# Optimization experiments

Measured on AMD Instinct MI355X. Metric: run time of the kernel, lower is better.

The kernel has to match this reference:

```python
import jax, jax.numpy as jnp
import numpy as np

HEADS = 16
DIM_HEAD = 32
WSZ = 7
DIM = 512
INNER = HEADS * DIM_HEAD
LN_EPS = 1e-5


def setup_inputs() -> dict:
    key = jax.random.key(0)
    ks = jax.random.split(key, 9)
    b, H, W = 16, 56, 56
    x = jax.random.normal(ks[0], (b, DIM, H, W), dtype=jnp.float32)
    w_qkv = jax.random.normal(ks[1], (INNER * 3, DIM), dtype=jnp.float32) * (DIM ** -0.5)
    window_tokens = jax.random.normal(ks[2], (DIM,), dtype=jnp.float32)
    ln_w = jnp.ones((DIM_HEAD,), dtype=jnp.float32)
    ln_b = jnp.zeros((DIM_HEAD,), dtype=jnp.float32)
    w_qk = jax.random.normal(ks[3], (INNER * 2, INNER), dtype=jnp.float32) * (INNER ** -0.5)
    b_qk = jnp.zeros((INNER * 2,), dtype=jnp.float32)
    w_out = jax.random.normal(ks[4], (DIM, INNER), dtype=jnp.float32) * (INNER ** -0.5)
    b_out = jnp.zeros((DIM,), dtype=jnp.float32)
    return {"x": x, "w_qkv": w_qkv, "window_tokens": window_tokens,
            "ln_w": ln_w, "ln_b": ln_b, "w_qk": w_qk, "b_qk": b_qk,
            "w_out": w_out, "b_out": b_out}


def reference(x, w_qkv, window_tokens, ln_w, ln_b, w_qk, b_qk, w_out, b_out):
    b, c, H, W = x.shape
    h, d, wsz = HEADS, DIM_HEAD, WSZ
    X, Y = H // wsz, W // wsz
    nw = X * Y            # number of windows per image
    n = wsz * wsz         # tokens per window (49)
    scale = d ** -0.5

    # b c (X w1) (Y w2) -> (b X Y) c (w1 w2)
    xw = x.reshape(b, c, X, wsz, Y, wsz).transpose(0, 2, 4, 1, 3, 5).reshape(b * nw, c, n)
    wt = jnp.broadcast_to(window_tokens[None, :, None], (b * nw, c, 1))
    xc = jnp.concatenate([wt, xw], axis=-1)                 # [BW, c, n+1]

    qkv = jnp.einsum('oc,bcn->bon', w_qkv, xc)              # 1x1 conv, no bias
    q, k, v = jnp.split(qkv, 3, axis=1)
    def to_heads(t):
        return t.reshape(t.shape[0], h, d, n + 1).transpose(0, 1, 3, 2)  # [BW,h,n+1,d]
    q, k, v = to_heads(q), to_heads(k), to_heads(v)

    dots = jnp.einsum('bhid,bhjd->bhij', q * scale, k)      # [BW,h,50,50]
    attn = jax.nn.softmax(dots, axis=-1)
    out = jnp.einsum('bhij,bhjd->bhid', attn, v)            # [BW,h,50,d]

    wtok = out[:, :, 0].reshape(b, nw, h, d).transpose(0, 2, 1, 3)          # [b,h,nw,d]
    wfm = out[:, :, 1:].reshape(b, nw, h, n, d).transpose(0, 2, 1, 3, 4)    # [b,h,nw,n,d]

    # window_tokens_to_qk: LayerNorm(d) -> GELU -> conv1d(inner, 2*inner)
    mu = wtok.mean(-1, keepdims=True)
    var = wtok.var(-1, keepdims=True)
    normed = (wtok - mu) / jnp.sqrt(var + LN_EPS) * ln_w + ln_b
    g = jax.nn.gelu(normed, approximate=False)
    gf = g.transpose(0, 1, 3, 2).reshape(b, h * d, nw)      # b h n c -> b (h c) n
    qk = jnp.einsum('oc,bcn->bon', w_qk, gf) + b_qk[None, :, None]
    qk = qk.reshape(b, h, 2 * d, nw).transpose(0, 1, 3, 2)  # [b,h,nw,2d]
    w_q, w_k = qk[..., :d], qk[..., d:]

    w_dots = jnp.einsum('bhid,bhjd->bhij', w_q * scale, w_k)  # [b,h,nw,nw]
    w_attn = jax.nn.softmax(w_dots, axis=-1)
    agg = jnp.einsum('bhij,bhjnd->bhind', w_attn, wfm)        # [b,h,nw,n,d]

    # b h (X Y) (w1 w2) d -> b (h d) (X w1) (Y w2)
    fmap = agg.reshape(b, h, X, Y, wsz, wsz, d).transpose(0, 1, 6, 2, 4, 3, 5).reshape(b, h * d, H, W)
    return jnp.einsum('oc,bchw->bohw', w_out, fmap) + b_out[None, :, None, None]
```

## Files before the change

kernel.cpp:

```cpp
#include <hip/hip_runtime.h>
#include <math.h>

#define SCALE_D 0.17677669529663687f

typedef __attribute__((ext_vector_type(8))) short short8;
typedef __attribute__((ext_vector_type(4))) float f32x4;

__device__ __forceinline__ unsigned short f2bf(float f) {
  unsigned u = __builtin_bit_cast(unsigned, f);
  unsigned r = u + 0x7FFF + ((u >> 16) & 1);
  return (unsigned short)(r >> 16);
}
__device__ __forceinline__ float bf2f(unsigned short h) {
  unsigned u = ((unsigned)h) << 16;
  return __builtin_bit_cast(float, u);
}
__device__ __forceinline__ void gload16(const void* g, void* l) {
  __builtin_amdgcn_global_load_lds((const __attribute__((address_space(1))) unsigned int*)g,
                                   (__attribute__((address_space(3))) unsigned int*)l,
                                   16, 0, 0);
}

__global__ __launch_bounds__(256) void k_split(const float* __restrict__ src,
                                               unsigned short* __restrict__ hi,
                                               unsigned short* __restrict__ lo, int n) {
  int i = blockIdx.x * 256 + threadIdx.x;
  if (i < n) {
    float v = src[i];
    unsigned short h = f2bf(v);
    hi[i] = h;
    lo[i] = f2bf(v - bf2f(h));
  }
}

__global__ __launch_bounds__(256) void k_build_xcT(const float* __restrict__ x,
                                                   const float* __restrict__ wtok,
                                                   unsigned short* __restrict__ Thi,
                                                   unsigned short* __restrict__ Tlo,
                                                   int bb0) {
  const int cblk = blockIdx.x;
  const int h    = blockIdx.y;
  const int bbL  = blockIdx.z;
  const int bb   = bb0 + bbL;
  const int tid  = threadIdx.x;
  const int c0   = cblk * 64;
  if (h == 56) {
    for (int e = tid; e < 4096; e += 256) {
      int wl = e >> 6, cl = e & 63;
      float v = wtok[c0 + cl];
      unsigned short hv = f2bf(v);
      long idx = ((long)(bbL * 64 + wl) * 50) * 512 + c0 + cl;
      Thi[idx] = hv;
      Tlo[idx] = f2bf(v - bf2f(hv));
    }
    return;
  }
  __shared__ unsigned short shi[64][57], slo[64][57];
  const int Xw = h / 7, r7 = h % 7;
  for (int e = tid; e < 3584; e += 256) {
    int cl = e / 56, w = e - cl * 56;
    float v = x[((long)(bb * 512 + c0 + cl) * 56 + h) * 56 + w];
    unsigned short hv = f2bf(v);
    shi[cl][w] = hv;
    slo[cl][w] = f2bf(v - bf2f(hv));
  }
  __syncthreads();
  for (int e = tid; e < 3584; e += 256) {
    int row = e >> 6, cl = e & 63;
    int Yw = row / 7, c7 = row - Yw * 7;
    long trow = (long)(bbL * 64 + Xw * 8 + Yw) * 50 + 1 + r7 * 7 + c7;
    Thi[trow * 512 + c0 + cl] = shi[cl][row];
    Tlo[trow * 512 + c0 + cl] = slo[cl][row];
  }
}

template <int PACK>
__global__ __launch_bounds__(256, 2) void k_gemm_mfma(
    const unsigned short* __restrict__ Ahi, const unsigned short* __restrict__ Alo,
    const unsigned short* __restrict__ Bhi, const unsigned short* __restrict__ Blo,
    float* __restrict__ C, const float* __restrict__ bias,
    int NC, int brow_stride, long c_stride) {
  __shared__ unsigned short lds[2][4][128][32];
  const int tid = threadIdx.x;
  const int wv = tid >> 6, lane = tid & 63;

  const int gy = gridDim.y;
  const int nwg = gridDim.x * gy;
  int hw = blockIdx.y * gridDim.x + blockIdx.x;
  int flat;
  {
    int q = nwg >> 3, r = nwg & 7;
    int xcd = hw & 7, k = hw >> 3;
    int start = (xcd < r) ? xcd * (q + 1) : r * (q + 1) + (xcd - r) * q;
    flat = start + k;
  }
  const int bx = flat / gy, by = flat % gy;
  const int m0 = by * 128, n0 = bx * 128;
  const long brow0 = (long)blockIdx.z * brow_stride + n0;
  C += (long)blockIdx.z * c_stride;

  const int wr = wv >> 1, wc = wv & 1;
  const int lr = lane & 15, kb = lane >> 4;
  const int srow = lane >> 2, sju = lane & 3;
  const int sswz = (sju ^ ((srow >> 1) & 3)) * 8;
  const int rswz = (lr >> 1) & 3;

  f32x4 acc[4][4];
#pragma unroll
  for (int i = 0; i < 4; ++i)
#pragma unroll
    for (int j = 0; j < 4; ++j) {
      f32x4 z = {0.f, 0.f, 0.f, 0.f};
      acc[i][j] = z;
    }

  auto STAGE = [&](int buf, int k0) {
#pragma unroll
    for (int it = 0; it < 2; ++it) {
      const int rloc = (wv * 2 + it) * 16;
      const int r = rloc + srow;
      const long ga = (long)(m0 + r) * 512 + k0 + sswz;
      gload16(Ahi + ga, &lds[buf][0][rloc][0]);
      gload16(Alo + ga, &lds[buf][1][rloc][0]);
      const long gb = (brow0 + r) * 512 + k0 + sswz;
      gload16(Bhi + gb, &lds[buf][2][rloc][0]);
      gload16(Blo + gb, &lds[buf][3][rloc][0]);
    }
  };

  STAGE(0, 0);
  int cur = 0;
  for (int t = 0; t < 16; ++t) {
    if (t < 15) STAGE(cur ^ 1, (t + 1) * 32);
    if (t < 15) {
      asm volatile("s_waitcnt vmcnt(8)" ::: "memory");
    } else {
      asm volatile("s_waitcnt vmcnt(0)" ::: "memory");
    }
    __builtin_amdgcn_s_barrier();
    asm volatile("" ::: "memory");
    short8 ah[4], al[4], bh[4], bl[4];
#pragma unroll
    for (int f = 0; f < 4; ++f) {
      int ra = wr * 64 + f * 16 + lr;
      int ca = (kb ^ rswz) * 8;
      ah[f] = *(const short8*)&lds[cur][0][ra][ca];
      al[f] = *(const short8*)&lds[cur][1][ra][ca];
      int rb = wc * 64 + f * 16 + lr;
      bh[f] = *(const short8*)&lds[cur][2][rb][ca];
      bl[f] = *(const short8*)&lds[cur][3][rb][ca];
    }
#pragma unroll
    for (int i = 0; i < 4; ++i)
#pragma unroll
      for (int j = 0; j < 4; ++j) {
        acc[i][j] = __builtin_amdgcn_mfma_f32_16x16x32_bf16(ah[i], bh[j], acc[i][j], 0, 0, 0);
        acc[i][j] = __builtin_amdgcn_mfma_f32_16x16x32_bf16(ah[i], bl[j], acc[i][j], 0, 0, 0);
        acc[i][j] = __builtin_amdgcn_mfma_f32_16x16x32_bf16(al[i], bh[j], acc[i][j], 0, 0, 0);
      }
    asm volatile("s_waitcnt lgkmcnt(0)" ::: "memory");
    __builtin_amdgcn_s_barrier();
    asm volatile("" ::: "memory");
    cur ^= 1;
  }

#pragma unroll
  for (int i = 0; i < 4; ++i)
#pragma unroll
    for (int nf = 0; nf < 4; ++nf) {
      int col = n0 + wc * 64 + nf * 16 + lr;
      if (col < NC) {
#pragma unroll
        for (int j4 = 0; j4 < 4; ++j4) {
          int row = m0 + wr * 64 + i * 16 + kb * 4 + j4;
          float v = acc[i][nf][j4];
          if (PACK) {
            unsigned short h = f2bf(v);
            unsigned short l = f2bf(v - bf2f(h));
            ((unsigned*)C)[(long)row * NC + col] = (unsigned)h | ((unsigned)l << 16);
          } else {
            C[(long)row * NC + col] = v + (bias ? bias[row] : 0.f);
          }
        }
      }
    }
}

__global__ __launch_bounds__(256) void k_attn1_mfma(const unsigned* __restrict__ QKV,
                                                    float* __restrict__ OUT1, int w0) {
  __shared__ unsigned short P[4][16][72];
  const int tid = threadIdx.x;
  const int wv = tid >> 6, lane = tid & 63;
  const int idx = blockIdx.x * 4 + wv;
  const int wl = idx >> 4, h = idx & 15;
  const int lr = lane & 15, kb = lane >> 4;
  const long tb = (long)wl * 50;

  short8 kh[4], kl[4];
#pragma unroll
  for (int jt = 0; jt < 4; ++jt) {
#pragma unroll
    for (int e = 0; e < 8; ++e) {
      unsigned u = QKV[(long)(512 + h * 32 + kb * 8 + e) * 12800 + tb + jt * 16 + lr];
      kh[jt][e] = (short)(u & 0xFFFF);
      kl[jt][e] = (short)(u >> 16);
    }
  }
  short8 vh[2][2], vl[2][2];
#pragma unroll
  for (int ddt = 0; ddt < 2; ++ddt)
#pragma unroll
    for (int ks = 0; ks < 2; ++ks) {
      const long vb = (long)(1024 + h * 32 + ddt * 16 + lr) * 12800 + tb + ks * 32 + kb * 8;
#pragma unroll
      for (int e = 0; e < 8; ++e) {
        int j = ks * 32 + kb * 8 + e;
        unsigned u = (j < 50) ? QKV[vb + e] : 0u;
        vh[ddt][ks][e] = (short)(u & 0xFFFF);
        vl[ddt][ks][e] = (short)(u >> 16);
      }
    }

  const long ob = (long)((w0 + wl) * 16 + h) * 1600;

  for (int it = 0; it < 4; ++it) {
    short8 qh, ql;
#pragma unroll
    for (int e = 0; e < 8; ++e) {
      unsigned u = QKV[(long)(h * 32 + kb * 8 + e) * 12800 + tb + it * 16 + lr];
      qh[e] = (short)(u & 0xFFFF);
      ql[e] = (short)(u >> 16);
    }
    f32x4 s[4];
#pragma unroll
    for (int jt = 0; jt < 4; ++jt) {
      f32x4 z = {0.f, 0.f, 0.f, 0.f};
      s[jt] = z;
      s[jt] = __builtin_amdgcn_mfma_f32_16x16x32_bf16(qh, kh[jt], s[jt], 0, 0, 0);
      s[jt] = __builtin_amdgcn_mfma_f32_16x16x32_bf16(qh, kl[jt], s[jt], 0, 0, 0);
      s[jt] = __builtin_amdgcn_mfma_f32_16x16x32_bf16(ql, kh[jt], s[jt], 0, 0, 0);
#pragma unroll
      for (int r = 0; r < 4; ++r) s[jt][r] *= SCALE_D;
    }
    if (lr >= 2) {
#pragma unroll
      for (int r = 0; r < 4; ++r) s[3][r] = -1e30f;
    }
    float ex[4][4], rinv[4];
#pragma unroll
    for (int r = 0; r < 4; ++r) {
      float m = fmaxf(fmaxf(s[0][r], s[1][r]), fmaxf(s[2][r], s[3][r]));
      m = fmaxf(m, __shfl_xor(m, 1));
      m = fmaxf(m, __shfl_xor(m, 2));
      m = fmaxf(m, __shfl_xor(m, 4));
      m = fmaxf(m, __shfl_xor(m, 8));
      float sm = 0.f;
#pragma unroll
      for (int jt = 0; jt < 4; ++jt) {
        ex[jt][r] = __expf(s[jt][r] - m);
        sm += ex[jt][r];
      }
      sm += __shfl_xor(sm, 1);
      sm += __shfl_xor(sm, 2);
      sm += __shfl_xor(sm, 4);
      sm += __shfl_xor(sm, 8);
      rinv[r] = 1.f / sm;
    }
#pragma unroll
    for (int jt = 0; jt < 4; ++jt)
#pragma unroll
      for (int r = 0; r < 4; ++r)
        P[wv][kb * 4 + r][jt * 16 + lr] = f2bf(ex[jt][r] * rinv[r]);
    short8 pa0 = *(const short8*)&P[wv][lr][kb * 8];
    short8 pa1 = *(const short8*)&P[wv][lr][32 + kb * 8];
    f32x4 o[2];
#pragma unroll
    for (int ddt = 0; ddt < 2; ++ddt) {
      f32x4 z = {0.f, 0.f, 0.f, 0.f};
      o[ddt] = z;
      o[ddt] = __builtin_amdgcn_mfma_f32_16x16x32_bf16(pa0, vh[ddt][0], o[ddt], 0, 0, 0);
      o[ddt] = __builtin_amdgcn_mfma_f32_16x16x32_bf16(pa0, vl[ddt][0], o[ddt], 0, 0, 0);
      o[ddt] = __builtin_amdgcn_mfma_f32_16x16x32_bf16(pa1, vh[ddt][1], o[ddt], 0, 0, 0);
      o[ddt] = __builtin_amdgcn_mfma_f32_16x16x32_bf16(pa1, vl[ddt][1], o[ddt], 0, 0, 0);
    }
#pragma unroll
    for (int ddt = 0; ddt < 2; ++ddt)
#pragma unroll
      for (int r = 0; r < 4; ++r) {
        int i = it * 16 + kb * 4 + r;
        if (i < 50) OUT1[ob + i * 32 + ddt * 16 + lr] = o[ddt][r];
      }
  }
}

__global__ __launch_bounds__(256) void k_gemm(const float* __restrict__ A,
                                              const float* __restrict__ Bg,
                                              float* __restrict__ C,
                                              const float* __restrict__ bias,
                                              int M, int N, int K, long sB, long sC) {
  Bg += (long)blockIdx.z * sB;
  C  += (long)blockIdx.z * sC;
  __shared__ __align__(16) float As[32][132];
  __shared__ __align__(16) float Bs[32][132];
  const int tid = threadIdx.x;
  const int tx = tid & 15, ty = tid >> 4;
  const int m0 = blockIdx.y * 128, n0 = blockIdx.x * 128;

  float acc[8][8];
#pragma unroll
  for (int q = 0; q < 8; ++q)
#pragma unroll
    for (int r = 0; r < 8; ++r) acc[q][r] = 0.f;

  for (int k0 = 0; k0 < K; k0 += 32) {
#pragma unroll
    for (int it = 0; it < 4; ++it) {
      int idx = tid + it * 256;
      int row = idx >> 3, c4 = idx & 7;
      const float4 f = *(const float4*)&A[(long)(m0 + row) * K + k0 + c4 * 4];
      As[c4 * 4 + 0][row] = f.x;
      As[c4 * 4 + 1][row] = f.y;
      As[c4 * 4 + 2][row] = f.z;
      As[c4 * 4 + 3][row] = f.w;
    }
#pragma unroll
    for (int it = 0; it < 4; ++it) {
      int idx = tid + it * 256;
      int row = idx >> 5, c4 = idx & 31;
      int col = n0 + c4 * 4;
      float4 f;
      if (col + 3 < N) {
        f = *(const float4*)&Bg[(long)(k0 + row) * N + col];
      } else {
        f.x = (col + 0 < N) ? Bg[(long)(k0 + row) * N + col + 0] : 0.f;
        f.y = (col + 1 < N) ? Bg[(long)(k0 + row) * N + col + 1] : 0.f;
        f.z = (col + 2 < N) ? Bg[(long)(k0 + row) * N + col + 2] : 0.f;
        f.w = (col + 3 < N) ? Bg[(long)(k0 + row) * N + col + 3] : 0.f;
      }
      *(float4*)&Bs[row][c4 * 4] = f;
    }
    __syncthreads();
#pragma unroll
    for (int kk = 0; kk < 32; ++kk) {
      const float4 a0 = *(const float4*)&As[kk][ty * 8];
      const float4 a1 = *(const float4*)&As[kk][ty * 8 + 4];
      const float4 b0 = *(const float4*)&Bs[kk][tx * 8];
      const float4 b1 = *(const float4*)&Bs[kk][tx * 8 + 4];
      const float am[8] = {a0.x, a0.y, a0.z, a0.w, a1.x, a1.y, a1.z, a1.w};
      const float bn[8] = {b0.x, b0.y, b0.z, b0.w, b1.x, b1.y, b1.z, b1.w};
#pragma unroll
      for (int q = 0; q < 8; ++q)
#pragma unroll
        for (int r = 0; r < 8; ++r) acc[q][r] += am[q] * bn[r];
    }
    __syncthreads();
  }

#pragma unroll
  for (int q = 0; q < 8; ++q) {
    int m = m0 + ty * 8 + q;
    float bv = bias ? bias[m] : 0.f;
#pragma unroll
    for (int half = 0; half < 8; half += 4) {
      int col = n0 + tx * 8 + half;
#pragma unroll
      for (int rr = 0; rr < 4; ++rr)
        if (col + rr < N) C[(long)m * N + col + rr] = acc[q][half + rr] + bv;
    }
  }
}

__global__ __launch_bounds__(256) void k_ln_gelu(const float* __restrict__ OUT1,
                                                 const float* __restrict__ lnw,
                                                 const float* __restrict__ lnb,
                                                 float* __restrict__ G) {
  const int tid = threadIdx.x;
  const int r = blockIdx.x * 8 + (tid >> 5);
  const int l = tid & 31;
  const int bb = r >> 10, hh = (r >> 6) & 15, wp = r & 63;
  float v = OUT1[((long)((bb * 64 + wp) * 16 + hh)) * 1600 + l];
  float s = v, s2 = v * v;
#pragma unroll
  for (int o = 16; o >= 1; o >>= 1) {
    s += __shfl_xor(s, o, 32);
    s2 += __shfl_xor(s2, o, 32);
  }
  float mu = s * (1.f / 32.f);
  float var = s2 * (1.f / 32.f) - mu * mu;
  float xn = (v - mu) * rsqrtf(var + 1e-5f) * lnw[l] + lnb[l];
  float g = 0.5f * xn * (1.f + erff(xn * 0.70710678118654752f));
  G[((long)(bb * 512 + hh * 32 + l)) * 64 + wp] = g;
}

__global__ __launch_bounds__(256) void k_attn2_agg(const float* __restrict__ QK,
                                                   const float* __restrict__ OUT1,
                                                   float* __restrict__ AGG) {
  const int bh = blockIdx.x;
  const int bb = bh >> 4, hh = bh & 15;
  const int tid = threadIdx.x;
  __shared__ float wqs[64 * 33], wks[64 * 33];
  __shared__ float sd[64 * 65];
  __shared__ __align__(16) float pt[64 * 68];
  __shared__ float smx[64], ssum[64];

  for (int t = tid; t < 2048; t += 256) {
    int dd = t >> 6, i = t & 63;
    wqs[i * 33 + dd] = QK[((long)(bb * 1024 + hh * 64 + dd)) * 64 + i] * SCALE_D;
    wks[i * 33 + dd] = QK[((long)(bb * 1024 + hh * 64 + 32 + dd)) * 64 + i];
  }
  __syncthreads();
  for (int t = tid; t < 4096; t += 256) {
    int i = t >> 6, j = t & 63;
    float s = 0.f;
#pragma unroll
    for (int dd = 0; dd < 32; ++dd) s += wqs[i * 33 + dd] * wks[j * 33 + dd];
    sd[i * 65 + j] = s;
  }
  __syncthreads();
  if (tid < 64) {
    float mx = -1e30f;
    for (int j = 0; j < 64; ++j) mx = fmaxf(mx, sd[tid * 65 + j]);
    float sm = 0.f;
    for (int j = 0; j < 64; ++j) sm += expf(sd[tid * 65 + j] - mx);
    smx[tid] = mx;
    ssum[tid] = 1.f / sm;
  }
  __syncthreads();
  for (int t = tid; t < 4096; t += 256) {
    int i = t >> 6, j = t & 63;
    pt[j * 68 + i] = expf(sd[i * 65 + j] - smx[i]) * ssum[i];
  }
  __syncthreads();

  const int ih = tid >> 7, jl = tid & 127;
  const int jd = blockIdx.y * 512 + jl * 4;
  const bool act = jd < 1568;
  float4 acc[32];
#pragma unroll
  for (int i = 0; i < 32; ++i) acc[i] = make_float4(0.f, 0.f, 0.f, 0.f);
  for (int wp = 0; wp < 64; ++wp) {
    float4 pv = make_float4(0.f, 0.f, 0.f, 0.f);
    if (act) pv = *(const float4*)&OUT1[((long)((bb * 64 + wp) * 16 + hh)) * 1600 + 32 + jd];
#pragma unroll
    for (int ii = 0; ii < 32; ii += 4) {
      const float4 p = *(const float4*)&pt[wp * 68 + ih * 32 + ii];
      acc[ii + 0].x += p.x * pv.x; acc[ii + 0].y += p.x * pv.y;
      acc[ii + 0].z += p.x * pv.z; acc[ii + 0].w += p.x * pv.w;
      acc[ii + 1].x += p.y * pv.x; acc[ii + 1].y += p.y * pv.y;
      acc[ii + 1].z += p.y * pv.z; acc[ii + 1].w += p.y * pv.w;
      acc[ii + 2].x += p.z * pv.x; acc[ii + 2].y += p.z * pv.y;
      acc[ii + 2].z += p.z * pv.z; acc[ii + 2].w += p.z * pv.w;
      acc[ii + 3].x += p.w * pv.x; acc[ii + 3].y += p.w * pv.y;
      acc[ii + 3].z += p.w * pv.z; acc[ii + 3].w += p.w * pv.w;
    }
  }
  if (act) {
    const long base = (long)bh * 100352 + jd;
#pragma unroll
    for (int i = 0; i < 32; ++i)
      *(float4*)&AGG[base + (long)(ih * 32 + i) * 1568] = acc[i];
  }
}

__global__ __launch_bounds__(256) void k_fmap_T(const float* __restrict__ AGG,
                                                unsigned short* __restrict__ Thi,
                                                unsigned short* __restrict__ Tlo) {
  const int wp = blockIdx.x, bb = blockIdx.y;
  const int Xw = wp >> 3, Yw = wp & 7;
  const int c = threadIdx.x * 2;
  const int hh = c >> 5, d0 = c & 31;
  const long abase = ((long)(bb * 16 + hh) * 64 + wp) * 1568;
  for (int j = 0; j < 49; ++j) {
    float v0 = AGG[abase + j * 32 + d0];
    float v1 = AGG[abase + j * 32 + d0 + 1];
    int hw = (Xw * 7 + j / 7) * 56 + Yw * 7 + j % 7;
    long t = ((long)bb * 3200 + hw) * 512 + c;
    unsigned short h0 = f2bf(v0), h1 = f2bf(v1);
    unsigned short l0 = f2bf(v0 - bf2f(h0)), l1 = f2bf(v1 - bf2f(h1));
    *(unsigned*)&Thi[t] = (unsigned)h0 | ((unsigned)h1 << 16);
    *(unsigned*)&Tlo[t] = (unsigned)l0 | ((unsigned)l1 << 16);
  }
}

__global__ __launch_bounds__(256) void k_padzero(unsigned short* __restrict__ Thi,
                                                 unsigned short* __restrict__ Tlo) {
  const int bb = blockIdx.x;
  for (int e = threadIdx.x; e < 32768; e += 256) {
    long idx = ((long)bb * 3200 + 3136) * 512 + e;
    Thi[idx] = 0;
    Tlo[idx] = 0;
  }
}

extern "C" void kernel_launch(void* const* d_in, const int* in_sizes, int n_in,
                              void* d_out, int out_size, void* d_ws, size_t ws_size,
                              hipStream_t stream) {
  const float* x     = (const float*)d_in[0];
  const float* w_qkv = (const float*)d_in[1];
  const float* wt    = (const float*)d_in[2];
  const float* lnw   = (const float*)d_in[3];
  const float* lnb   = (const float*)d_in[4];
  const float* w_qk  = (const float*)d_in[5];
  const float* b_qk  = (const float*)d_in[6];
  const float* w_out = (const float*)d_in[7];
  const float* b_out = (const float*)d_in[8];
  float* out = (float*)d_out;
  float* ws  = (float*)d_ws;

  float* OUT1 = ws;
  float* AUX  = ws + 26214400L;
  unsigned short* XThi = (unsigned short*)(ws + 21233664L);
  unsigned short* XTlo = XThi + 6553600L;
  float* G  = AUX;
  float* QK = AUX + 524288L;
  unsigned short* WOhi = (unsigned short*)AUX;
  unsigned short* WOlo = WOhi + 262144L;
  unsigned short* FThi = (unsigned short*)ws;
  unsigned short* FTlo = FThi + 26214400L;

  unsigned* QKVc = (unsigned*)d_out;
  unsigned short* Whi = (unsigned short*)(out + 19660800L);
  unsigned short* Wlo = Whi + 786432L;
  float* AGG = out;

  k_split<<<3072, 256, 0, stream>>>(w_qkv, Whi, Wlo, 786432);
  for (int c = 0; c < 4; ++c) {
    k_build_xcT<<<dim3(8, 57, 4), 256, 0, stream>>>(x, wt, XThi, XTlo, c * 4);
    k_gemm_mfma<1><<<dim3(100, 12, 1), 256, 0, stream>>>(Whi, Wlo, XThi, XTlo,
                                                         (float*)QKVc, nullptr,
                                                         12800, 0, 0);
    k_attn1_mfma<<<1024, 256, 0, stream>>>(QKVc, OUT1, c * 256);
  }
  k_ln_gelu<<<2048, 256, 0, stream>>>(OUT1, lnw, lnb, G);
  k_gemm<<<dim3(1, 8, 16), 256, 0, stream>>>(w_qk, G, QK, b_qk,
                                             1024, 64, 512, 512L * 64, 1024L * 64);
  k_split<<<1024, 256, 0, stream>>>(w_out, WOhi, WOlo, 262144);
  k_attn2_agg<<<dim3(256, 4, 1), 256, 0, stream>>>(QK, OUT1, AGG);
  k_fmap_T<<<dim3(64, 16), 256, 0, stream>>>(AGG, FThi, FTlo);
  k_padzero<<<16, 256, 0, stream>>>(FThi, FTlo);
  k_gemm_mfma<0><<<dim3(25, 4, 16), 256, 0, stream>>>(WOhi, WOlo, FThi, FTlo, out,
                                                      b_out, 3136, 3200, 512L * 3136);
}
```

Before: 834.6 us.

## Compute window-aggregation matmul with split-bf16 MFMA instead of scalar FMA

The aggregation of window features by the window-attention matrix (64x64 times 64x1568 per batch-head) now runs on bf16 MFMA. Both operands are split into hi/lo bf16 parts and three MFMAs approximate fp32 accuracy. V tiles are transposed into LDS 64 columns at a time, and the grid drops from 4 to 2 column blocks per head. This targets the scalar FMA cost of the old register-tiled loop, at the price of extra split and transpose work, more barriers, and scattered 4-byte output stores.

```diff
diff --git a/kernel.cpp b/kernel.cpp
--- a/kernel.cpp
+++ b/kernel.cpp
@@ -392,16 +392,21 @@
   G[((long)(bb * 512 + hh * 32 + l)) * 64 + wp] = g;
 }
 
-__global__ __launch_bounds__(256) void k_attn2_agg(const float* __restrict__ QK,
-                                                   const float* __restrict__ OUT1,
-                                                   float* __restrict__ AGG) {
+__global__ __launch_bounds__(256) void k_attn2_mfma(const float* __restrict__ QK,
+                                                    const float* __restrict__ OUT1,
+                                                    float* __restrict__ AGG) {
   const int bh = blockIdx.x;
   const int bb = bh >> 4, hh = bh & 15;
   const int tid = threadIdx.x;
+  const int wv = tid >> 6, lane = tid & 63;
+  const int lr = lane & 15, kb = lane >> 4;
+  const int wr = wv >> 1, wc = wv & 1;
+
   __shared__ float wqs[64 * 33], wks[64 * 33];
   __shared__ float sd[64 * 65];
-  __shared__ __align__(16) float pt[64 * 68];
   __shared__ float smx[64], ssum[64];
+  __shared__ __align__(16) unsigned short PAh[64][72], PAl[64][72];
+  __shared__ __align__(16) unsigned short VTh[64][72], VTl[64][72];
 
   for (int t = tid; t < 2048; t += 256) {
     int dd = t >> 6, i = t & 63;
@@ -428,37 +433,60 @@
   __syncthreads();
   for (int t = tid; t < 4096; t += 256) {
     int i = t >> 6, j = t & 63;
-    pt[j * 68 + i] = expf(sd[i * 65 + j] - smx[i]) * ssum[i];
+    float p = expf(sd[i * 65 + j] - smx[i]) * ssum[i];
+    unsigned short h = f2bf(p);
+    PAh[i][j] = h;
+    PAl[i][j] = f2bf(p - bf2f(h));
   }
   __syncthreads();
 
-  const int ih = tid >> 7, jl = tid & 127;
-  const int jd = blockIdx.y * 512 + jl * 4;
-  const bool act = jd < 1568;
-  float4 acc[32];
-#pragma unroll
-  for (int i = 0; i < 32; ++i) acc[i] = make_float4(0.f, 0.f, 0.f, 0.f);
-  for (int wp = 0; wp < 64; ++wp) {
-    float4 pv = make_float4(0.f, 0.f, 0.f, 0.f);
-    if (act) pv = *(const float4*)&OUT1[((long)((bb * 64 + wp) * 16 + hh)) * 1600 + 32 + jd];
-#pragma unroll
-    for (int ii = 0; ii < 32; ii += 4) {
-      const float4 p = *(const float4*)&pt[wp * 68 + ih * 32 + ii];
-      acc[ii + 0].x += p.x * pv.x; acc[ii + 0].y += p.x * pv.y;
-      acc[ii + 0].z += p.x * pv.z; acc[ii + 0].w += p.x * pv.w;
-      acc[ii + 1].x += p.y * pv.x; acc[ii + 1].y += p.y * pv.y;
-      acc[ii + 1].z += p.y * pv.z; acc[ii + 1].w += p.y * pv.w;
-      acc[ii + 2].x += p.z * pv.x; acc[ii + 2].y += p.z * pv.y;
-      acc[ii + 2].z += p.z * pv.z; acc[ii + 2].w += p.z * pv.w;
-      acc[ii + 3].x += p.w * pv.x; acc[ii + 3].y += p.w * pv.y;
-      acc[ii + 3].z += p.w * pv.z; acc[ii + 3].w += p.w * pv.w;
-    }
-  }
-  if (act) {
-    const long base = (long)bh * 100352 + jd;
-#pragma unroll
-    for (int i = 0; i < 32; ++i)
-      *(float4*)&AGG[base + (long)(ih * 32 + i) * 1568] = acc[i];
+  const int jstart = blockIdx.y * 13;
+  const int ntiles = (blockIdx.y == 0) ? 13 : 12;
+  const int swp = tid >> 2, sq = tid & 3;
+  const long vbase = ((long)((bb * 64 + swp) * 16 + hh)) * 1600 + 32;
+  const long abase = (long)bh * 100352;
+
+  for (int tt = 0; tt < ntiles; ++tt) {
+    const int jt = jstart + tt;
+    const int jd0 = jt * 64;
+    const int JT = (jt == 24) ? 32 : 64;
+    for (int jj = 0; jj < (JT >> 4); ++jj) {
+      const float4 v4 = *(const float4*)&OUT1[vbase + jd0 + jj * 16 + sq * 4];
+#pragma unroll
+      for (int e = 0; e < 4; ++e) {
+        int jl = jj * 16 + sq * 4 + e;
+        float v = (e == 0) ? v4.x : (e == 1) ? v4.y : (e == 2) ? v4.z : v4.w;
+        unsigned short h = f2bf(v);
+        VTh[jl][swp] = h;
+        VTl[jl][swp] = f2bf(v - bf2f(h));
+      }
+    }
+    __syncthreads();
+#pragma unroll
+    for (int mt = 0; mt < 2; ++mt) {
+      const int i0 = wr * 32 + mt * 16;
+#pragma unroll
+      for (int nt = 0; nt < 2; ++nt) {
+        const int jl0 = wc * 32 + nt * 16;
+        if (jl0 < JT) {
+          f32x4 acc = {0.f, 0.f, 0.f, 0.f};
+#pragma unroll
+          for (int ks = 0; ks < 2; ++ks) {
+            const short8 pah = *(const short8*)&PAh[i0 + lr][ks * 32 + kb * 8];
+            const short8 pal = *(const short8*)&PAl[i0 + lr][ks * 32 + kb * 8];
+            const short8 vth = *(const short8*)&VTh[jl0 + lr][ks * 32 + kb * 8];
+            const short8 vtl = *(const short8*)&VTl[jl0 + lr][ks * 32 + kb * 8];
+            acc = __builtin_amdgcn_mfma_f32_16x16x32_bf16(pah, vth, acc, 0, 0, 0);
+            acc = __builtin_amdgcn_mfma_f32_16x16x32_bf16(pah, vtl, acc, 0, 0, 0);
+            acc = __builtin_amdgcn_mfma_f32_16x16x32_bf16(pal, vth, acc, 0, 0, 0);
+          }
+#pragma unroll
+          for (int r = 0; r < 4; ++r)
+            AGG[abase + (long)(i0 + kb * 4 + r) * 1568 + jd0 + jl0 + lr] = acc[r];
+        }
+      }
+    }
+    __syncthreads();
   }
 }
 
@@ -535,7 +563,7 @@
   k_gemm<<<dim3(1, 8, 16), 256, 0, stream>>>(w_qk, G, QK, b_qk,
                                              1024, 64, 512, 512L * 64, 1024L * 64);
   k_split<<<1024, 256, 0, stream>>>(w_out, WOhi, WOlo, 262144);
-  k_attn2_agg<<<dim3(256, 4, 1), 256, 0, stream>>>(QK, OUT1, AGG);
+  k_attn2_mfma<<<dim3(256, 2, 1), 256, 0, stream>>>(QK, OUT1, AGG);
   k_fmap_T<<<dim3(64, 16), 256, 0, stream>>>(AGG, FThi, FTlo);
   k_padzero<<<16, 256, 0, stream>>>(FThi, FTlo);
   k_gemm_mfma<0><<<dim3(25, 4, 16), 256, 0, stream>>>(WOhi, WOlo, FThi, FTlo, out,
```

Result: faster. 788.9 us (-5.5%).
